# Kernel tuning notes

Hardware: AMD Instinct MI355X
Metric: run time of the kernel (lower is better)

The kernel has to match this reference:

```python
import jax, jax.numpy as jnp
import numpy as np

B, S, H, D = 8, 1024, 1024, 64

def setup_inputs() -> dict:
    key = jax.random.key(0)
    ks = jax.random.split(key, 8)
    return {
        "query": jax.random.normal(ks[0], (B, S, H), jnp.float32),
        "key": jax.random.normal(ks[1], (B, S, H), jnp.float32),
        "value": jax.random.normal(ks[2], (B, S, H), jnp.float32),
        "Wq": jax.random.normal(ks[3], (H, D), jnp.float32) * 0.02,
        "bq": jnp.zeros((D,), jnp.float32),
        "Wk": jax.random.normal(ks[4], (H, D), jnp.float32) * 0.02,
        "bk": jnp.zeros((D,), jnp.float32),
        "Wv": jax.random.normal(ks[5], (H, D), jnp.float32) * 0.02,
        "bv": jnp.zeros((D,), jnp.float32),
        "k_bias_matrix": jax.random.normal(ks[6], (S, S, D), jnp.float32) * 0.02,
        "v_bias_matrix": jax.random.normal(ks[7], (S, S, D), jnp.float32) * 0.02,
        "mask": jnp.ones((B, S), jnp.int32),
    }

def reference(query, key, value, Wq, bq, Wk, bk, Wv, bv, k_bias_matrix, v_bias_matrix, mask):
    # Linear projections: [B,S,H] -> [B,S,D]
    q = query @ Wq + bq
    k = key @ Wk + bk
    v = value @ Wv + bv
    # Standard content score + Shaw relative-position key bias score
    attn_1 = jnp.einsum('bqd,bkd->bqk', q, k)
    attn_2 = jnp.einsum('bqd,qkd->bqk', q, k_bias_matrix)
    scores = (attn_1 + attn_2) / jnp.sqrt(jnp.float32(D))
    scores = jnp.where(mask[:, None, :] == 0, jnp.float32(-1e9), scores)
    w = jax.nn.softmax(scores, axis=-1)  # [B,S,S]
    values_1 = jnp.einsum('bqk,bkd->bqd', w, v)
    values_2 = jnp.einsum('bqk,qkd->bqd', w, v_bias_matrix)
    return values_1 + values_2
```

## Files before the change

kernel.cpp:

```cpp
#include <hip/hip_runtime.h>
#include <hip/hip_bf16.h>
#include <cstdint>
#include <cstddef>

#define NB 8
#define NS 1024
#define NH 1024
#define ND 64

typedef __attribute__((ext_vector_type(8))) short bf8_t;
typedef __attribute__((ext_vector_type(4))) float f32x4;
typedef __attribute__((ext_vector_type(4))) short short4v;

__device__ __forceinline__ short f2bfs(float x) {
    union { __hip_bfloat16 h; short s; } u;
    u.h = __float2bfloat16(x);
    return u.s;
}
__device__ __forceinline__ float bf2f(unsigned short h) {
    return __uint_as_float(((unsigned int)h) << 16);
}
__device__ __forceinline__ bf8_t pack_bf8(float4 a, float4 b) {
    bf8_t r;
    r[0] = f2bfs(a.x); r[1] = f2bfs(a.y); r[2] = f2bfs(a.z); r[3] = f2bfs(a.w);
    r[4] = f2bfs(b.x); r[5] = f2bfs(b.y); r[6] = f2bfs(b.z); r[7] = f2bfs(b.w);
    return r;
}

#define QP_OFF  0
#define KP_OFF  524288
#define VPT_OFF 1048576
#define S1_OFF  1572864
#define WT_OFF  9961472

__global__ __launch_bounds__(256, 8) void wcvt_kernel(
    const float* __restrict__ Wq, const float* __restrict__ Wk,
    const float* __restrict__ Wv, short* __restrict__ wt)
{
    const int p = blockIdx.y;
    const int n = blockIdx.x;
    const float* W = (p == 0) ? Wq : (p == 1) ? Wk : Wv;
    const int k0 = threadIdx.x * 4;
    short4v pk;
    #pragma unroll
    for (int i = 0; i < 4; ++i) pk[i] = f2bfs(W[(size_t)(k0 + i) * ND + n]);
    *(short4v*)&wt[((size_t)p * 64 + n) * 1024 + k0] = pk;
}

__global__ __launch_bounds__(256, 3) void proj_kernel(
    const float* __restrict__ qin, const float* __restrict__ kin, const float* __restrict__ vin,
    const short* __restrict__ wt,
    const float* __restrict__ bq, const float* __restrict__ bk, const float* __restrict__ bv,
    short* __restrict__ ws_s)
{
    __shared__ float red[2][16][68];

    const int p = blockIdx.y;
    const float* A    = (p == 0) ? qin : (p == 1) ? kin : vin;
    const float* bias = (p == 0) ? bq  : (p == 1) ? bk  : bv;

    const int t = threadIdx.x;
    const int wv = t >> 6, l = t & 63, lr = l & 15, lg = l >> 4;
    const int rt = wv >> 1, kh = wv & 1;
    const int rw = blockIdx.x * 32 + rt * 16;

    const short* wtp = wt + ((size_t)p * 64) * 1024 + kh * 512;
    const float* ab  = A + (size_t)(rw + lr) * NH + kh * 512;

    f32x4 acc[4];
    #pragma unroll
    for (int n = 0; n < 4; ++n) acc[n] = (f32x4){0.f, 0.f, 0.f, 0.f};

    #pragma unroll 2
    for (int ch = 0; ch < 4; ++ch) {
        #pragma unroll
        for (int s = 0; s < 4; ++s) {
            const int off = ch * 128 + s * 32 + lg * 8;
            bf8_t af = pack_bf8(*(const float4*)&ab[off], *(const float4*)&ab[off + 4]);
            #pragma unroll
            for (int n = 0; n < 4; ++n) {
                bf8_t bf = *(const bf8_t*)&wtp[(size_t)(n * 16 + lr) * 1024 + off];
                acc[n] = __builtin_amdgcn_mfma_f32_16x16x32_bf16(af, bf, acc[n], 0, 0, 0);
            }
        }
    }

    if (kh) {
        #pragma unroll
        for (int n = 0; n < 4; ++n)
            #pragma unroll
            for (int r = 0; r < 4; ++r)
                red[rt][lg * 4 + r][n * 16 + lr] = acc[n][r];
    }
    __syncthreads();
    if (!kh) {
        if (p < 2) {
            short* dst = ws_s + ((p == 0) ? QP_OFF : KP_OFF);
            const float sc = (p == 0) ? 0.125f : 1.0f;
            #pragma unroll
            for (int n = 0; n < 4; ++n) {
                const float bs = bias[n * 16 + lr];
                #pragma unroll
                for (int r = 0; r < 4; ++r) {
                    float v = acc[n][r] + red[rt][lg * 4 + r][n * 16 + lr] + bs;
                    dst[(size_t)(rw + lg * 4 + r) * ND + n * 16 + lr] = f2bfs(v * sc);
                }
            }
        } else {
            short* vpT = ws_s + VPT_OFF;
            const int b = rw >> 10;
            const int sbase = (rw & 1023) + lg * 4;
            #pragma unroll
            for (int n = 0; n < 4; ++n) {
                const float bs = bias[n * 16 + lr];
                short4v pk;
                #pragma unroll
                for (int r = 0; r < 4; ++r)
                    pk[r] = f2bfs(acc[n][r] + red[rt][lg * 4 + r][n * 16 + lr] + bs);
                *(short4v*)&vpT[((size_t)b * 64 + n * 16 + lr) * NS + sbase] = pk;
            }
        }
    }
}

__global__ __launch_bounds__(256, 4) void scores_c_kernel(
    const short* __restrict__ ws_s, short* __restrict__ s1)
{
    const short* qp = ws_s + QP_OFF;
    const short* kp = ws_s + KP_OFF;
    const int t = threadIdx.x;
    const int wv = t >> 6, l = t & 63, lr = l & 15, lg = l >> 4;
    const int q0 = blockIdx.y * 16;
    const int k0 = blockIdx.x * 64 + wv * 16;

    #pragma unroll
    for (int b = 0; b < 8; ++b) {
        const short* ap = &qp[((size_t)b * NS + q0 + lr) * ND + lg * 8];
        const short* bp = &kp[((size_t)b * NS + k0 + lr) * ND + lg * 8];
        bf8_t a0 = *(const bf8_t*)ap;
        bf8_t a1 = *(const bf8_t*)(ap + 32);
        bf8_t b0 = *(const bf8_t*)bp;
        bf8_t b1 = *(const bf8_t*)(bp + 32);
        f32x4 acc = {0.f, 0.f, 0.f, 0.f};
        acc = __builtin_amdgcn_mfma_f32_16x16x32_bf16(a0, b0, acc, 0, 0, 0);
        acc = __builtin_amdgcn_mfma_f32_16x16x32_bf16(a1, b1, acc, 0, 0, 0);
        #pragma unroll
        for (int r = 0; r < 4; ++r)
            s1[((size_t)b * NS + q0 + lg * 4 + r) * NS + k0 + lr] = f2bfs(acc[r]);
    }
}

__global__ __launch_bounds__(256, 4) void sm_kernel(
    const short* __restrict__ ws_s,
    short* __restrict__ s1,
    const float* __restrict__ kbias,
    const int* __restrict__ mask)
{
    __shared__ __align__(16) short Sb[8][1032];

    const short* qp = ws_s + QP_OFF;
    const int q = blockIdx.x, t = threadIdx.x;
    const int wv = t >> 6, l = t & 63, lr = l & 15, lg = l >> 4;

    {
        const bf8_t aq0 = *(const bf8_t*)&qp[((size_t)(lr & 7) * NS + q) * ND + lg * 8];
        const bf8_t aq1 = *(const bf8_t*)&qp[((size_t)(lr & 7) * NS + q) * ND + 32 + lg * 8];
        const float* kbq = kbias + (size_t)q * NS * ND;

        #pragma unroll 4
        for (int it = 0; it < 16; ++it) {
            const int k0 = wv * 256 + it * 16;
            const float* kb = &kbq[(size_t)(k0 + lr) * ND + lg * 8];
            bf8_t b0 = pack_bf8(*(const float4*)kb, *(const float4*)(kb + 4));
            bf8_t b1 = pack_bf8(*(const float4*)(kb + 32), *(const float4*)(kb + 36));
            f32x4 acc = {0.f, 0.f, 0.f, 0.f};
            acc = __builtin_amdgcn_mfma_f32_16x16x32_bf16(aq0, b0, acc, 0, 0, 0);
            acc = __builtin_amdgcn_mfma_f32_16x16x32_bf16(aq1, b1, acc, 0, 0, 0);
            if (lg < 2) {
                #pragma unroll
                for (int r = 0; r < 4; ++r)
                    Sb[lg * 4 + r][k0 + lr] = f2bfs(acc[r]);
            }
        }
    }
    __syncthreads();

    {
        const int b = t >> 5, idx = t & 31;
        const int kk = idx * 32;
        short* r1 = s1 + ((size_t)b * NS + q) * NS + kk;
        const int* mb = mask + b * NS + kk;
        const float LOG2E = 1.4426950408889634f;

        float x[32];
        float m = -3.0e38f;
        #pragma unroll
        for (int c = 0; c < 4; ++c) {
            uint4 a4 = *(const uint4*)&r1[8 * c];
            uint4 b4 = *(const uint4*)&Sb[b][kk + 8 * c];
            int4 m0 = *(const int4*)&mb[8 * c];
            int4 m1 = *(const int4*)&mb[8 * c + 4];
            const unsigned short* ap = (const unsigned short*)&a4;
            const unsigned short* bp = (const unsigned short*)&b4;
            const int* mp = (const int*)&m0;
            const int* mq = (const int*)&m1;
            #pragma unroll
            for (int j = 0; j < 8; ++j) {
                float v = bf2f(ap[j]) + bf2f(bp[j]);
                const int mvv = (j < 4) ? mp[j] : mq[j - 4];
                v = (mvv == 0) ? -1e9f : v;
                x[8 * c + j] = v;
                m = fmaxf(m, v);
            }
        }
        #pragma unroll
        for (int off = 1; off < 32; off <<= 1) m = fmaxf(m, __shfl_xor(m, off, 32));

        float lsum = 0.f;
        #pragma unroll
        for (int j = 0; j < 32; ++j) { x[j] = exp2f((x[j] - m) * LOG2E); lsum += x[j]; }
        #pragma unroll
        for (int off = 1; off < 32; off <<= 1) lsum += __shfl_xor(lsum, off, 32);
        const float il = 1.0f / fmaxf(lsum, 1e-30f);

        unsigned short wv16[32];
        #pragma unroll
        for (int j = 0; j < 32; ++j) wv16[j] = (unsigned short)f2bfs(x[j] * il);

        #pragma unroll
        for (int c = 0; c < 4; ++c)
            *(uint4*)&r1[8 * c] = *(const uint4*)&wv16[8 * c];
    }
}

__global__ __launch_bounds__(256, 4) void v2_kernel(
    const short* __restrict__ s1,
    const float* __restrict__ vbias,
    float* __restrict__ out)
{
    __shared__ __align__(16) short Wt[8][1024];
    __shared__ __align__(16) float otile[4][8][64];

    const int q = blockIdx.x, t = threadIdx.x;
    const int wv = t >> 6, l = t & 63;

    {
        const int rr = t >> 5;
        const int c0 = (t & 31) * 32;
        const short* src = &s1[((size_t)rr * NS + q) * NS + c0];
        #pragma unroll
        for (int j = 0; j < 4; ++j)
            *(uint4*)&Wt[rr][c0 + j * 8] = *(const uint4*)&src[j * 8];
    }
    __syncthreads();

    const int kq = l >> 4, dq = l & 15;
    const int kw = wv * 256;
    const float* vbq = vbias + (size_t)q * NS * ND;

    float4 av[8];
    #pragma unroll
    for (int b = 0; b < 8; ++b) av[b] = make_float4(0.f, 0.f, 0.f, 0.f);

    for (int i = 0; i < 16; ++i) {
        const int kb = kw + i * 16 + kq * 4;
        short4v w4[8];
        #pragma unroll
        for (int b = 0; b < 8; ++b) w4[b] = *(const short4v*)&Wt[b][kb];
        float4 vb[4];
        #pragma unroll
        for (int j = 0; j < 4; ++j)
            vb[j] = *(const float4*)&vbq[(size_t)(kb + j) * ND + 4 * dq];
        #pragma unroll
        for (int j = 0; j < 4; ++j) {
            #pragma unroll
            for (int b = 0; b < 8; ++b) {
                const float wgt = bf2f((unsigned short)w4[b][j]);
                av[b].x += wgt * vb[j].x; av[b].y += wgt * vb[j].y;
                av[b].z += wgt * vb[j].z; av[b].w += wgt * vb[j].w;
            }
        }
    }
    #pragma unroll
    for (int b = 0; b < 8; ++b) {
        #pragma unroll
        for (int off = 16; off <= 32; off <<= 1) {
            av[b].x += __shfl_xor(av[b].x, off, 64);
            av[b].y += __shfl_xor(av[b].y, off, 64);
            av[b].z += __shfl_xor(av[b].z, off, 64);
            av[b].w += __shfl_xor(av[b].w, off, 64);
        }
    }
    if (l < 16) {
        #pragma unroll
        for (int b = 0; b < 8; ++b)
            *(float4*)&otile[wv][b][4 * l] = av[b];
    }
    __syncthreads();

    if (t < 128) {
        const int b = t >> 4, dd = (t & 15) * 4;
        float4 s = make_float4(0.f, 0.f, 0.f, 0.f);
        #pragma unroll
        for (int w4i = 0; w4i < 4; ++w4i) {
            float4 r = *(const float4*)&otile[w4i][b][dd];
            s.x += r.x; s.y += r.y; s.z += r.z; s.w += r.w;
        }
        *(float4*)&out[((size_t)b * NS + q) * ND + dd] = s;
    }
}

__global__ __launch_bounds__(256, 2) void v1_kernel(
    const short* __restrict__ ws_s, const short* __restrict__ w,
    float* __restrict__ out)
{
    const short* vpT = ws_s + VPT_OFF;
    const int t = threadIdx.x, wv = t >> 6, l = t & 63, lr = l & 15, lg = l >> 4;
    const int b = blockIdx.y;
    const int q0 = blockIdx.x * 16;

    f32x4 acc[4];
    #pragma unroll
    for (int j = 0; j < 4; ++j) acc[j] = (f32x4){0.f, 0.f, 0.f, 0.f};

    const short* arow = &w[((size_t)b * NS + q0 + lr) * NS + lg * 8];
    const short* brow = &vpT[((size_t)b * ND + wv * 16 + lr) * NS + lg * 8];
    #pragma unroll 8
    for (int ch = 0; ch < 32; ++ch) {
        bf8_t a  = *(const bf8_t*)(arow + ch * 32);
        bf8_t bb = *(const bf8_t*)(brow + ch * 32);
        acc[ch & 3] = __builtin_amdgcn_mfma_f32_16x16x32_bf16(a, bb, acc[ch & 3], 0, 0, 0);
    }
    f32x4 s;
    #pragma unroll
    for (int r = 0; r < 4; ++r) s[r] = acc[0][r] + acc[1][r] + acc[2][r] + acc[3][r];

    #pragma unroll
    for (int r = 0; r < 4; ++r) {
        float* op = &out[((size_t)b * NS + q0 + lg * 4 + r) * ND + wv * 16 + lr];
        *op = *op + s[r];
    }
}

extern "C" void kernel_launch(void* const* d_in, const int* in_sizes, int n_in,
                              void* d_out, int out_size, void* d_ws, size_t ws_size,
                              hipStream_t stream) {
    (void)in_sizes; (void)n_in; (void)out_size; (void)ws_size;
    const float* query = (const float*)d_in[0];
    const float* key   = (const float*)d_in[1];
    const float* value = (const float*)d_in[2];
    const float* Wq    = (const float*)d_in[3];
    const float* bq    = (const float*)d_in[4];
    const float* Wk    = (const float*)d_in[5];
    const float* bk    = (const float*)d_in[6];
    const float* Wv    = (const float*)d_in[7];
    const float* bv    = (const float*)d_in[8];
    const float* kbias = (const float*)d_in[9];
    const float* vbias = (const float*)d_in[10];
    const int*   mask  = (const int*)d_in[11];
    short* ws_s = (short*)d_ws;
    short* s1 = ws_s + S1_OFF;
    short* wt = ws_s + WT_OFF;
    float* outp = (float*)d_out;

    wcvt_kernel<<<dim3(64, 3), 256, 0, stream>>>(Wq, Wk, Wv, wt);
    proj_kernel<<<dim3(256, 3), 256, 0, stream>>>(query, key, value, wt, bq, bk, bv, ws_s);
    scores_c_kernel<<<dim3(16, 64), 256, 0, stream>>>(ws_s, s1);
    sm_kernel<<<1024, 256, 0, stream>>>(ws_s, s1, kbias, mask);
    v2_kernel<<<1024, 256, 0, stream>>>(s1, vbias, outp);
    v1_kernel<<<dim3(64, 8), 256, 0, stream>>>(ws_s, s1, outp);
}
```

Measured before the change: 202.3 us.

## Split bias-score and bias-value kernels over key halves, separate softmax pass

The fused bias-score plus softmax kernel is split. A bias-score kernel now runs over two key halves per query and writes a bf16 score buffer, and a separate row-wise softmax kernel combines the content and bias scores. The v_bias kernel is likewise split across two key halves, writes partial outputs to workspace, and a combine kernel adds them before v1 accumulates. This doubles the block count for the large kbias/vbias streaming kernels to improve occupancy and latency hiding. The cost is extra kernel launches and extra global traffic for the intermediate score and partial-output buffers.

```diff
diff --git a/kernel.cpp b/kernel.cpp
--- a/kernel.cpp
+++ b/kernel.cpp
@@ -27,11 +27,13 @@
     return r;
 }
 
-#define QP_OFF  0
-#define KP_OFF  524288
-#define VPT_OFF 1048576
-#define S1_OFF  1572864
-#define WT_OFF  9961472
+#define QP_OFF   0
+#define KP_OFF   524288
+#define VPT_OFF  1048576
+#define S1_OFF   1572864
+#define WT_OFF   9961472
+#define S2_OFF   10158080
+#define POUT_OFF 18546688
 
 __global__ __launch_bounds__(256, 8) void wcvt_kernel(
     const float* __restrict__ Wq, const float* __restrict__ Wk,
@@ -150,27 +152,26 @@
     }
 }
 
-__global__ __launch_bounds__(256, 4) void sm_kernel(
+__global__ __launch_bounds__(256, 4) void sm2_kernel(
     const short* __restrict__ ws_s,
-    short* __restrict__ s1,
-    const float* __restrict__ kbias,
-    const int* __restrict__ mask)
-{
-    __shared__ __align__(16) short Sb[8][1032];
+    short* __restrict__ s2,
+    const float* __restrict__ kbias)
+{
+    __shared__ __align__(16) short Sb[8][520];
 
     const short* qp = ws_s + QP_OFF;
-    const int q = blockIdx.x, t = threadIdx.x;
+    const int q = blockIdx.x, kh = blockIdx.y, t = threadIdx.x;
     const int wv = t >> 6, l = t & 63, lr = l & 15, lg = l >> 4;
 
     {
         const bf8_t aq0 = *(const bf8_t*)&qp[((size_t)(lr & 7) * NS + q) * ND + lg * 8];
         const bf8_t aq1 = *(const bf8_t*)&qp[((size_t)(lr & 7) * NS + q) * ND + 32 + lg * 8];
-        const float* kbq = kbias + (size_t)q * NS * ND;
+        const float* kbq = kbias + (size_t)q * NS * ND + (size_t)kh * 512 * ND;
 
         #pragma unroll 4
-        for (int it = 0; it < 16; ++it) {
-            const int k0 = wv * 256 + it * 16;
-            const float* kb = &kbq[(size_t)(k0 + lr) * ND + lg * 8];
+        for (int it = 0; it < 8; ++it) {
+            const int kl0 = wv * 128 + it * 16;
+            const float* kb = &kbq[(size_t)(kl0 + lr) * ND + lg * 8];
             bf8_t b0 = pack_bf8(*(const float4*)kb, *(const float4*)(kb + 4));
             bf8_t b1 = pack_bf8(*(const float4*)(kb + 32), *(const float4*)(kb + 36));
             f32x4 acc = {0.f, 0.f, 0.f, 0.f};
@@ -179,98 +180,109 @@
             if (lg < 2) {
                 #pragma unroll
                 for (int r = 0; r < 4; ++r)
-                    Sb[lg * 4 + r][k0 + lr] = f2bfs(acc[r]);
+                    Sb[lg * 4 + r][kl0 + lr] = f2bfs(acc[r]);
             }
         }
     }
     __syncthreads();
 
     {
-        const int b = t >> 5, idx = t & 31;
-        const int kk = idx * 32;
-        short* r1 = s1 + ((size_t)b * NS + q) * NS + kk;
-        const int* mb = mask + b * NS + kk;
-        const float LOG2E = 1.4426950408889634f;
-
-        float x[32];
-        float m = -3.0e38f;
-        #pragma unroll
-        for (int c = 0; c < 4; ++c) {
-            uint4 a4 = *(const uint4*)&r1[8 * c];
-            uint4 b4 = *(const uint4*)&Sb[b][kk + 8 * c];
-            int4 m0 = *(const int4*)&mb[8 * c];
-            int4 m1 = *(const int4*)&mb[8 * c + 4];
-            const unsigned short* ap = (const unsigned short*)&a4;
-            const unsigned short* bp = (const unsigned short*)&b4;
-            const int* mp = (const int*)&m0;
-            const int* mq = (const int*)&m1;
-            #pragma unroll
-            for (int j = 0; j < 8; ++j) {
-                float v = bf2f(ap[j]) + bf2f(bp[j]);
-                const int mvv = (j < 4) ? mp[j] : mq[j - 4];
-                v = (mvv == 0) ? -1e9f : v;
-                x[8 * c + j] = v;
-                m = fmaxf(m, v);
-            }
-        }
-        #pragma unroll
-        for (int off = 1; off < 32; off <<= 1) m = fmaxf(m, __shfl_xor(m, off, 32));
-
-        float lsum = 0.f;
-        #pragma unroll
-        for (int j = 0; j < 32; ++j) { x[j] = exp2f((x[j] - m) * LOG2E); lsum += x[j]; }
-        #pragma unroll
-        for (int off = 1; off < 32; off <<= 1) lsum += __shfl_xor(lsum, off, 32);
-        const float il = 1.0f / fmaxf(lsum, 1e-30f);
-
-        unsigned short wv16[32];
-        #pragma unroll
-        for (int j = 0; j < 32; ++j) wv16[j] = (unsigned short)f2bfs(x[j] * il);
-
-        #pragma unroll
-        for (int c = 0; c < 4; ++c)
-            *(uint4*)&r1[8 * c] = *(const uint4*)&wv16[8 * c];
-    }
+        #pragma unroll
+        for (int c = 0; c < 2; ++c) {
+            const int idx = t + 256 * c;
+            const int row = idx >> 6;
+            const int col = (idx & 63) * 8;
+            *(uint4*)&s2[((size_t)q * NB + row) * NS + kh * 512 + col] =
+                *(const uint4*)&Sb[row][col];
+        }
+    }
+}
+
+__global__ __launch_bounds__(256, 4) void smx_kernel(
+    short* __restrict__ s1, const short* __restrict__ s2,
+    const int* __restrict__ mask)
+{
+    const int t = threadIdx.x, wv = t >> 6, l = t & 63;
+    const int row = blockIdx.x * 4 + wv;
+    const int b = row >> 10, q = row & 1023;
+    short* r1 = s1 + (size_t)row * NS;
+    const short* r2 = s2 + ((size_t)q * NB + b) * NS;
+    const int* mb = mask + b * NS;
+    const float LOG2E = 1.4426950408889634f;
+    const int k0 = l * 16;
+
+    unsigned short sa[16], sb[16];
+    *(uint4*)&sa[0] = *(const uint4*)&r1[k0];
+    *(uint4*)&sa[8] = *(const uint4*)&r1[k0 + 8];
+    *(uint4*)&sb[0] = *(const uint4*)&r2[k0];
+    *(uint4*)&sb[8] = *(const uint4*)&r2[k0 + 8];
+    int mv[16];
+    #pragma unroll
+    for (int j = 0; j < 4; ++j) *(int4*)&mv[4 * j] = *(const int4*)&mb[k0 + 4 * j];
+
+    float x[16];
+    float m = -3.0e38f;
+    #pragma unroll
+    for (int j = 0; j < 16; ++j) {
+        float v = bf2f(sa[j]) + bf2f(sb[j]);
+        if (mv[j] == 0) v = -1e9f;
+        x[j] = v;
+        m = fmaxf(m, v);
+    }
+    #pragma unroll
+    for (int off = 1; off < 64; off <<= 1) m = fmaxf(m, __shfl_xor(m, off, 64));
+
+    float lsum = 0.f;
+    #pragma unroll
+    for (int j = 0; j < 16; ++j) { x[j] = exp2f((x[j] - m) * LOG2E); lsum += x[j]; }
+    #pragma unroll
+    for (int off = 1; off < 64; off <<= 1) lsum += __shfl_xor(lsum, off, 64);
+    const float il = 1.0f / fmaxf(lsum, 1e-30f);
+
+    #pragma unroll
+    for (int j = 0; j < 16; ++j) sa[j] = (unsigned short)f2bfs(x[j] * il);
+    *(uint4*)&r1[k0]     = *(const uint4*)&sa[0];
+    *(uint4*)&r1[k0 + 8] = *(const uint4*)&sa[8];
 }
 
 __global__ __launch_bounds__(256, 4) void v2_kernel(
     const short* __restrict__ s1,
     const float* __restrict__ vbias,
-    float* __restrict__ out)
-{
-    __shared__ __align__(16) short Wt[8][1024];
+    float* __restrict__ pout)
+{
+    __shared__ __align__(16) short Wt[8][512];
     __shared__ __align__(16) float otile[4][8][64];
 
-    const int q = blockIdx.x, t = threadIdx.x;
+    const int q = blockIdx.x, kh = blockIdx.y, t = threadIdx.x;
     const int wv = t >> 6, l = t & 63;
 
     {
         const int rr = t >> 5;
-        const int c0 = (t & 31) * 32;
-        const short* src = &s1[((size_t)rr * NS + q) * NS + c0];
-        #pragma unroll
-        for (int j = 0; j < 4; ++j)
-            *(uint4*)&Wt[rr][c0 + j * 8] = *(const uint4*)&src[j * 8];
+        const int c0 = (t & 31) * 16;
+        const short* src = &s1[((size_t)rr * NS + q) * NS + kh * 512 + c0];
+        *(uint4*)&Wt[rr][c0]     = *(const uint4*)&src[0];
+        *(uint4*)&Wt[rr][c0 + 8] = *(const uint4*)&src[8];
     }
     __syncthreads();
 
     const int kq = l >> 4, dq = l & 15;
-    const int kw = wv * 256;
-    const float* vbq = vbias + (size_t)q * NS * ND;
+    const int kw = wv * 128;
+    const float* vbq = vbias + (size_t)q * NS * ND + (size_t)kh * 512 * ND;
 
     float4 av[8];
     #pragma unroll
     for (int b = 0; b < 8; ++b) av[b] = make_float4(0.f, 0.f, 0.f, 0.f);
 
-    for (int i = 0; i < 16; ++i) {
+    #pragma unroll 2
+    for (int i = 0; i < 8; ++i) {
         const int kb = kw + i * 16 + kq * 4;
-        short4v w4[8];
-        #pragma unroll
-        for (int b = 0; b < 8; ++b) w4[b] = *(const short4v*)&Wt[b][kb];
         float4 vb[4];
         #pragma unroll
         for (int j = 0; j < 4; ++j)
             vb[j] = *(const float4*)&vbq[(size_t)(kb + j) * ND + 4 * dq];
+        short4v w4[8];
+        #pragma unroll
+        for (int b = 0; b < 8; ++b) w4[b] = *(const short4v*)&Wt[b][kb];
         #pragma unroll
         for (int j = 0; j < 4; ++j) {
             #pragma unroll
@@ -306,8 +318,19 @@
             float4 r = *(const float4*)&otile[w4i][b][dd];
             s.x += r.x; s.y += r.y; s.z += r.z; s.w += r.w;
         }
-        *(float4*)&out[((size_t)b * NS + q) * ND + dd] = s;
-    }
+        *(float4*)&pout[(size_t)kh * (NB * NS * ND) + ((size_t)b * NS + q) * ND + dd] = s;
+    }
+}
+
+__global__ __launch_bounds__(256, 8) void combine_kernel(
+    const float* __restrict__ pout, float* __restrict__ out)
+{
+    const size_t i = ((size_t)blockIdx.x * 256 + threadIdx.x) * 4;
+    float4 a = *(const float4*)&pout[i];
+    float4 b = *(const float4*)&pout[(size_t)NB * NS * ND + i];
+    float4 o;
+    o.x = a.x + b.x; o.y = a.y + b.y; o.z = a.z + b.z; o.w = a.w + b.w;
+    *(float4*)&out[i] = o;
 }
 
 __global__ __launch_bounds__(256, 2) void v1_kernel(
@@ -360,13 +383,17 @@
     const int*   mask  = (const int*)d_in[11];
     short* ws_s = (short*)d_ws;
     short* s1 = ws_s + S1_OFF;
+    short* s2 = ws_s + S2_OFF;
     short* wt = ws_s + WT_OFF;
+    float* pout = (float*)(ws_s + POUT_OFF);
     float* outp = (float*)d_out;
 
     wcvt_kernel<<<dim3(64, 3), 256, 0, stream>>>(Wq, Wk, Wv, wt);
     proj_kernel<<<dim3(256, 3), 256, 0, stream>>>(query, key, value, wt, bq, bk, bv, ws_s);
     scores_c_kernel<<<dim3(16, 64), 256, 0, stream>>>(ws_s, s1);
-    sm_kernel<<<1024, 256, 0, stream>>>(ws_s, s1, kbias, mask);
-    v2_kernel<<<1024, 256, 0, stream>>>(s1, vbias, outp);
+    sm2_kernel<<<dim3(1024, 2), 256, 0, stream>>>(ws_s, s2, kbias);
+    smx_kernel<<<2048, 256, 0, stream>>>(s1, s2, mask);
+    v2_kernel<<<dim3(1024, 2), 256, 0, stream>>>(s1, vbias, pout);
+    combine_kernel<<<512, 256, 0, stream>>>(pout, outp);
     v1_kernel<<<dim3(64, 8), 256, 0, stream>>>(ws_s, s1, outp);
 }
```

New measurement: 210.4 us. +4.0%, slower.
